# Performance work log

Measured on AMD Instinct MI355X. Metric: run time of the kernel, lower is better.

## Reference

```python
import jax, jax.numpy as jnp
import numpy as np

B_, L_, D_, R_, N_ = 8, 1024, 512, 32, 16  # batch, seq(in_channels), dim(=dim_inner), dt_rank, d_state


def setup_inputs() -> dict:
    key = jax.random.key(0)
    ks = jax.random.split(key, 8)
    s = lambda k, shape, scale: jax.random.normal(k, shape, dtype=jnp.float32) * scale
    inv = D_ ** -0.5
    return {
        "x": jax.random.uniform(ks[0], (B_, L_, D_), dtype=jnp.float32),
        "W1": s(ks[1], (D_, D_), inv), "b1": jnp.zeros((D_,), jnp.float32),
        "W2": s(ks[2], (D_, D_), inv), "b2": jnp.zeros((D_,), jnp.float32),
        "Wout": s(ks[3], (D_, D_), inv), "bout": jnp.zeros((D_,), jnp.float32),
        "conv_w": s(ks[4], (L_, L_, 3), (3 * L_) ** -0.5),  # Conv1d(L_, L_, k=3) weight (O,I,W)
        "conv_b": jnp.zeros((L_,), jnp.float32),
        "W_dbc": s(ks[5], (R_ + 2 * N_, D_), inv),          # deltaBC projection (no bias)
        "W_dt": s(ks[6], (D_, R_), R_ ** -0.5),             # dt_proj weight
        "b_dt": jnp.zeros((D_,), jnp.float32),
        "A_log": jnp.log(jnp.tile(jnp.arange(1, N_ + 1, dtype=jnp.float32), (D_, 1))),  # (D, N)
        "Dp": jnp.ones((D_,), jnp.float32),
    }


def _silu(v):
    return v * jax.nn.sigmoid(v)


def _selective_scan(u, delta, A, Bm, Cm, Dp):
    # u, delta: (b, l, d); A: (d, n); Bm, Cm: (b, l, n); Dp: (d,)
    dA = jnp.exp(jnp.einsum('bld,dn->bldn', delta, A))          # (b,l,d,n)
    dBu = jnp.einsum('bld,bln,bld->bldn', delta, Bm, u)          # (b,l,d,n)

    def step(h, inp):
        dA_t, dBu_t, C_t = inp                                   # (b,d,n),(b,d,n),(b,n)
        h = dA_t * h + dBu_t
        return h, jnp.einsum('bdn,bn->bd', h, C_t)

    h0 = jnp.zeros((u.shape[0], u.shape[2], A.shape[1]), u.dtype)
    _, ys = jax.lax.scan(step, h0, (dA.transpose(1, 0, 2, 3), dBu.transpose(1, 0, 2, 3), Cm.transpose(1, 0, 2)))
    return ys.transpose(1, 0, 2) + u * Dp                        # (b,l,d)


def reference(x, W1, b1, W2, b2, Wout, bout, conv_w, conv_b, W_dbc, W_dt, b_dt, A_log, Dp):
    skip = x
    x1 = x @ W1.T + b1                                            # proj_one
    x2 = x @ W2.T + b2                                            # proj_two
    # Conv1d over channel axis = L_ (dim 1), spatial axis = D_ (dim 2)
    x1 = jax.lax.conv_general_dilated(x1, conv_w, window_strides=(1,), padding=((1, 1),),
                                      dimension_numbers=('NCW', 'OIW', 'NCW')) + conv_b[None, :, None]
    x1 = _silu(x1)
    # SSM (zeta-style): deltaBC -> split -> dt_proj -> softplus -> selective scan
    dbc = x1 @ W_dbc.T                                            # (b,l,R+2N)
    delta = jax.nn.softplus(dbc[..., :R_] @ W_dt.T + b_dt)        # (b,l,d)
    Bm, Cm = dbc[..., R_:R_ + N_], dbc[..., R_ + N_:]
    A = -jnp.exp(A_log)
    y = _selective_scan(x1, delta, A, Bm, Cm, Dp)
    out = y * _silu(x2) + skip
    return out @ Wout.T + bout
```

## Files before the change

kernel.cpp:

```cpp
#include <hip/hip_runtime.h>
#include <hip/hip_bf16.h>

typedef __hip_bfloat16 bf16;
typedef __bf16 bf16x8 __attribute__((ext_vector_type(8)));
typedef float f32x4 __attribute__((ext_vector_type(4)));

static_assert(sizeof(bf16) == 2, "bf16 must be 2 bytes");

#define NC 32
#define CH 32
#define X1TP_BSTRIDE (514L * 1024)

__device__ __forceinline__ float silu_f(float v) { return v / (1.0f + __expf(-v)); }

__device__ __forceinline__ void gload16(const bf16* g, bf16* l) {
  __builtin_amdgcn_global_load_lds((const __attribute__((address_space(1))) void*)g,
                                   (__attribute__((address_space(3))) void*)l,
                                   16, 0, 0);
}

template <int N> __device__ __forceinline__ void wait_vm() {
  static_assert(N == 0 || N == 4 || N == 8 || N == 12, "add case");
  if constexpr (N == 0)       asm volatile("s_waitcnt vmcnt(0)" ::: "memory");
  else if constexpr (N == 4)  asm volatile("s_waitcnt vmcnt(4)" ::: "memory");
  else if constexpr (N == 8)  asm volatile("s_waitcnt vmcnt(8)" ::: "memory");
  else if constexpr (N == 12) asm volatile("s_waitcnt vmcnt(12)" ::: "memory");
}

__global__ __launch_bounds__(256) void prep_all(
    const float* __restrict__ x, const float* __restrict__ W1,
    const float* __restrict__ W2, const float* __restrict__ Wout,
    const float* __restrict__ Wdbc, const float* __restrict__ convw,
    bf16* __restrict__ xb, bf16* __restrict__ w1b, bf16* __restrict__ w2b,
    bf16* __restrict__ woutb, bf16* __restrict__ wdbcb,
    bf16* __restrict__ cws, bf16* __restrict__ x1tp) {
  const int gid = blockIdx.x * 256 + threadIdx.x;
  auto cvt4 = [](const float* src, bf16* dst, long q) {
    float4 v = *reinterpret_cast<const float4*>(src + q * 4);
    ushort4 s;
    s.x = __builtin_bit_cast(unsigned short, __float2bfloat16(v.x));
    s.y = __builtin_bit_cast(unsigned short, __float2bfloat16(v.y));
    s.z = __builtin_bit_cast(unsigned short, __float2bfloat16(v.z));
    s.w = __builtin_bit_cast(unsigned short, __float2bfloat16(v.w));
    *reinterpret_cast<ushort4*>(dst + q * 4) = s;
  };
  if (gid < 1048576) {
    cvt4(x, xb, gid);
  } else if (gid < 1114112) {
    cvt4(W1, w1b, gid - 1048576);
  } else if (gid < 1179648) {
    cvt4(W2, w2b, gid - 1114112);
  } else if (gid < 1245184) {
    cvt4(Wout, woutb, gid - 1179648);
  } else if (gid < 1253376) {
    cvt4(Wdbc, wdbcb, gid - 1245184);
  } else if (gid < 2301952) {
    long idx = gid - 1253376;
    int o = (int)(idx >> 10), i = (int)(idx & 1023);
    float a = convw[idx * 3], b = convw[idx * 3 + 1], c = convw[idx * 3 + 2];
    cws[(long)o * 3072 + i]        = __float2bfloat16(a);
    cws[(long)o * 3072 + 1024 + i] = __float2bfloat16(b);
    cws[(long)o * 3072 + 2048 + i] = __float2bfloat16(c);
  } else {
    int e = gid - 2301952;
    int b = e >> 11, rem = e & 2047;
    int r = rem >> 10, ii = rem & 1023;
    x1tp[(long)b * X1TP_BSTRIDE + (long)r * (513 * 1024) + ii] = __float2bfloat16(0.f);
  }
}

template <int EPI, int BM, int BN, int CONVB, int NBUF>
__device__ __forceinline__ void gemm_body(const bf16* __restrict__ A,
                                          const bf16* __restrict__ Bw,
                                          const float* __restrict__ bias,
                                          float* __restrict__ outf,
                                          bf16* __restrict__ outb,
                                          int M, int N, int K, int lda, int ldb,
                                          long sAz, long sBz, long sOz,
                                          int bx, int by, int z,
                                          bf16* As, bf16* Bs) {
  constexpr int BK = 64;
  constexpr int MI = BM / 32, WNF = BN / 32;
  constexpr int APW = BM / 32, BPW = BN / 32;
  constexpr int IPW = APW + BPW;

  const int tid = threadIdx.x;
  const int w = tid >> 6, l = tid & 63;
  const int wm = w >> 1, wn = w & 1;
  const int m0 = bx * BM, n0 = by * BN;
  const bf16* Ab = A + (long)z * sAz + (long)m0 * lda;
  const bf16* Bb = Bw + (long)z * sBz;

  const int lrow = l >> 3;
  const int lcol = (((l & 7) ^ (l >> 3)) << 3);

  auto stage = [&](int buf, int k0) {
#pragma unroll
    for (int j = 0; j < APW; ++j) {
      int iss = w * APW + j;
      int row = iss * 8 + lrow;
      gload16(Ab + (long)row * lda + k0 + lcol, &As[buf * BM * 64 + iss * 512]);
    }
#pragma unroll
    for (int j = 0; j < BPW; ++j) {
      int iss = w * BPW + j;
      int row = iss * 8 + lrow;
      const bf16* src;
      if (CONVB) src = Bb + (long)(n0 + row + (k0 >> 10)) * 1024 + (k0 & 1023) + lcol;
      else       src = Bb + (long)(n0 + row) * ldb + k0 + lcol;
      gload16(src, &Bs[buf * BN * 64 + iss * 512]);
    }
  };

  f32x4 acc[MI][WNF] = {};
  const int nt = K / BK;
  const int lr = l & 15;
  const int lko = (l >> 4) * 8;
  const int xorm = (lr & 7) << 3;

#pragma unroll
  for (int s = 0; s < NBUF - 1; ++s) stage(s, s * BK);
  for (int t = 0; t < nt; ++t) {
    const int cur = t % NBUF;
    if (t + NBUF - 1 < nt) {
      stage((t + NBUF - 1) % NBUF, (t + NBUF - 1) * BK);
      wait_vm<(NBUF - 1) * IPW>();
    } else {
      wait_vm<0>();
    }
    __builtin_amdgcn_s_barrier();
    __builtin_amdgcn_sched_barrier(0);
#pragma unroll
    for (int kk = 0; kk < 2; ++kk) {
      const int col = (lko + kk * 32) ^ xorm;
      bf16x8 af[MI], bfg[WNF];
#pragma unroll
      for (int mi = 0; mi < MI; ++mi)
        af[mi] = *reinterpret_cast<const bf16x8*>(
            &As[cur * BM * 64 + (wm * (BM / 2) + mi * 16 + lr) * 64 + col]);
#pragma unroll
      for (int ni = 0; ni < WNF; ++ni)
        bfg[ni] = *reinterpret_cast<const bf16x8*>(
            &Bs[cur * BN * 64 + (wn * (BN / 2) + ni * 16 + lr) * 64 + col]);
#pragma unroll
      for (int mi = 0; mi < MI; ++mi)
#pragma unroll
        for (int ni = 0; ni < WNF; ++ni)
          acc[mi][ni] = __builtin_amdgcn_mfma_f32_16x16x32_bf16(af[mi], bfg[ni], acc[mi][ni], 0, 0, 0);
    }
    __builtin_amdgcn_sched_barrier(0);
    __builtin_amdgcn_s_barrier();
  }

  const int lq = l >> 4;
#pragma unroll
  for (int mi = 0; mi < MI; ++mi) {
#pragma unroll
    for (int ni = 0; ni < WNF; ++ni) {
#pragma unroll
      for (int j = 0; j < 4; ++j) {
        int m = m0 + wm * (BM / 2) + mi * 16 + lq * 4 + j;
        int n = n0 + wn * (BN / 2) + ni * 16 + lr;
        float v = acc[mi][ni][j];
        if (EPI == 2) {
          v += bias[m];
          (outb + (long)z * sOz)[(long)m * N + n] = __float2bfloat16(silu_f(v));
        } else if (EPI == 3) {
          outf[(long)m * N + n] = v;
        } else if (EPI == 4) {
          v += bias[n];
          outf[(long)m * N + n] = v;
        } else if (EPI == 5) {
          v += bias[m];
          int b = n >> 10, li = n & 1023;
          outb[(long)b * X1TP_BSTRIDE + (long)(m + 1) * 1024 + li] = __float2bfloat16(v);
        } else {
          v += bias[n];
          outb[(long)m * N + n] = __float2bfloat16(silu_f(v));
        }
      }
    }
  }
}

template <int EPI, int BM, int BN, int CONVB, int NBUF, int GX, int GY>
__global__ __launch_bounds__(256) void gemm_nt(const bf16* __restrict__ A,
                                               const bf16* __restrict__ Bw,
                                               const float* __restrict__ bias,
                                               float* __restrict__ outf,
                                               bf16* __restrict__ outb,
                                               int M, int N, int K, int lda, int ldb,
                                               long sAz, long sBz, long sOz) {
  __shared__ __align__(16) bf16 As[NBUF * BM * 64];
  __shared__ __align__(16) bf16 Bs[NBUF * BN * 64];
  const int bid = (blockIdx.x & 7) * ((int)gridDim.x >> 3) + (blockIdx.x >> 3);
  const int by = bid % GY;
  const int bx = (bid / GY) % GX;
  const int z  = bid / (GX * GY);
  gemm_body<EPI, BM, BN, CONVB, NBUF>(A, Bw, bias, outf, outb, M, N, K, lda, ldb,
                                      sAz, sBz, sOz, bx, by, z, As, Bs);
}

__global__ __launch_bounds__(256) void gemm_dual(
    const bf16* __restrict__ w1b, const bf16* __restrict__ xb1,
    const float* __restrict__ b1, bf16* __restrict__ x1tp,
    const bf16* __restrict__ xb2, const bf16* __restrict__ w2b,
    const float* __restrict__ b2, bf16* __restrict__ x2g) {
  __shared__ __align__(16) bf16 As[2 * 128 * 64];
  __shared__ __align__(16) bf16 Bs[2 * 128 * 64];
  int bid = (blockIdx.x & 7) * 64 + (blockIdx.x >> 3);
  if (bid < 256) {
    int by = bid & 63, bx = bid >> 6;
    gemm_body<5, 128, 128, 0, 2>(w1b, xb1, b1, nullptr, x1tp, 512, 8192, 512, 512, 512,
                                 0, 0, 0, bx, by, 0, As, Bs);
  } else {
    bid -= 256;
    int by = bid & 3, bx = bid >> 2;
    gemm_body<6, 128, 128, 0, 2>(xb2, w2b, b2, nullptr, x2g, 8192, 512, 512, 512, 512,
                                 0, 0, 0, bx, by, 0, As, Bs);
  }
}

__global__ __launch_bounds__(256) void scan_p1(const bf16* __restrict__ u_bf,
                                               const float* __restrict__ dbc,
                                               const float* __restrict__ W_dt,
                                               const float* __restrict__ b_dt,
                                               const float* __restrict__ A_log,
                                               float* __restrict__ P,
                                               float* __restrict__ Q) {
  const int tid = threadIdx.x;
  const int d = blockIdx.x * 256 + tid;
  const int c = blockIdx.y, b = blockIdx.z;
  __shared__ float sD[CH][64];
  for (int i = tid; i < CH * 64; i += 256) {
    int tt = i >> 6, j = i & 63;
    sD[tt][j] = dbc[((long)b * 1024 + c * CH + tt) * 64 + j];
  }
  __syncthreads();
  float wdt[32];
#pragma unroll
  for (int r = 0; r < 32; r += 4) {
    float4 v = *reinterpret_cast<const float4*>(&W_dt[(long)d * 32 + r]);
    wdt[r] = v.x; wdt[r + 1] = v.y; wdt[r + 2] = v.z; wdt[r + 3] = v.w;
  }
  const float bd = b_dt[d];
  float Adn[16];
#pragma unroll
  for (int n = 0; n < 16; ++n) Adn[n] = -__expf(A_log[d * 16 + n]);
  float p[16], q[16];
#pragma unroll
  for (int n = 0; n < 16; ++n) { p[n] = 1.f; q[n] = 0.f; }
  const long rowb = (long)b * 1024 + c * CH;
  for (int tt = 0; tt < CH; ++tt) {
    float a = bd;
#pragma unroll
    for (int r = 0; r < 32; ++r) a = fmaf(sD[tt][r], wdt[r], a);
    float dv = fmaxf(a, 0.f) + log1pf(__expf(-fabsf(a)));
    float uv = __bfloat162float(u_bf[(rowb + tt) * 512 + d]);
    float s = dv * uv;
#pragma unroll
    for (int n = 0; n < 16; ++n) {
      float dA = __expf(dv * Adn[n]);
      p[n] *= dA;
      q[n] = fmaf(dA, q[n], s * sD[tt][32 + n]);
    }
  }
  float* Pp = P + ((long)b * NC + c) * 8192 + (long)d * 16;
  float* Qp = Q + ((long)b * NC + c) * 8192 + (long)d * 16;
#pragma unroll
  for (int n4 = 0; n4 < 4; ++n4) {
    *reinterpret_cast<float4*>(Pp + n4 * 4) = make_float4(p[n4*4], p[n4*4+1], p[n4*4+2], p[n4*4+3]);
    *reinterpret_cast<float4*>(Qp + n4 * 4) = make_float4(q[n4*4], q[n4*4+1], q[n4*4+2], q[n4*4+3]);
  }
}

__global__ __launch_bounds__(256) void scan_p2(const float* __restrict__ P,
                                               const float* __restrict__ Q,
                                               float* __restrict__ Hin) {
  const int dn = blockIdx.x * 256 + threadIdx.x;
  const int b = blockIdx.y;
  float h = 0.f;
#pragma unroll 4
  for (int c = 0; c < NC; ++c) {
    long idx = ((long)b * NC + c) * 8192 + dn;
    Hin[idx] = h;
    h = fmaf(P[idx], h, Q[idx]);
  }
}

__global__ __launch_bounds__(256) void scan_p3(const bf16* __restrict__ u_bf,
                                               const float* __restrict__ dbc,
                                               const float* __restrict__ W_dt,
                                               const float* __restrict__ b_dt,
                                               const float* __restrict__ A_log,
                                               const float* __restrict__ Dp,
                                               const bf16* __restrict__ x2g,
                                               const bf16* __restrict__ xres,
                                               const float* __restrict__ Hin,
                                               bf16* __restrict__ zb) {
  const int tid = threadIdx.x;
  const int d = blockIdx.x * 256 + tid;
  const int c = blockIdx.y, b = blockIdx.z;
  __shared__ float sD[CH][64];
  for (int i = tid; i < CH * 64; i += 256) {
    int tt = i >> 6, j = i & 63;
    sD[tt][j] = dbc[((long)b * 1024 + c * CH + tt) * 64 + j];
  }
  __syncthreads();
  float wdt[32];
#pragma unroll
  for (int r = 0; r < 32; r += 4) {
    float4 v = *reinterpret_cast<const float4*>(&W_dt[(long)d * 32 + r]);
    wdt[r] = v.x; wdt[r + 1] = v.y; wdt[r + 2] = v.z; wdt[r + 3] = v.w;
  }
  const float bd = b_dt[d];
  float Adn[16];
#pragma unroll
  for (int n = 0; n < 16; ++n) Adn[n] = -__expf(A_log[d * 16 + n]);
  float h[16];
  const float* Hp = Hin + ((long)b * NC + c) * 8192 + (long)d * 16;
#pragma unroll
  for (int n4 = 0; n4 < 4; ++n4) {
    float4 v = *reinterpret_cast<const float4*>(Hp + n4 * 4);
    h[n4*4] = v.x; h[n4*4+1] = v.y; h[n4*4+2] = v.z; h[n4*4+3] = v.w;
  }
  const float Dpv = Dp[d];
  const long rowb = (long)b * 1024 + c * CH;
  for (int tt = 0; tt < CH; ++tt) {
    long off = (rowb + tt) * 512 + d;
    float a = bd;
#pragma unroll
    for (int r = 0; r < 32; ++r) a = fmaf(sD[tt][r], wdt[r], a);
    float dv = fmaxf(a, 0.f) + log1pf(__expf(-fabsf(a)));
    float uv = __bfloat162float(u_bf[off]);
    float s = dv * uv;
    float y = uv * Dpv;
#pragma unroll
    for (int n = 0; n < 16; ++n) {
      float dA = __expf(dv * Adn[n]);
      h[n] = fmaf(dA, h[n], s * sD[tt][32 + n]);
      y = fmaf(h[n], sD[tt][48 + n], y);
    }
    float gate = __bfloat162float(x2g[off]);
    float xv = __bfloat162float(xres[off]);
    zb[off] = __float2bfloat16(fmaf(y, gate, xv));
  }
}

extern "C" void kernel_launch(void* const* d_in, const int* in_sizes, int n_in,
                              void* d_out, int out_size, void* d_ws, size_t ws_size,
                              hipStream_t stream) {
  (void)in_sizes; (void)n_in; (void)out_size; (void)ws_size;
  const float* x    = (const float*)d_in[0];
  const float* W1   = (const float*)d_in[1];
  const float* b1   = (const float*)d_in[2];
  const float* W2   = (const float*)d_in[3];
  const float* b2   = (const float*)d_in[4];
  const float* Wout = (const float*)d_in[5];
  const float* bout = (const float*)d_in[6];
  const float* convw = (const float*)d_in[7];
  const float* convb = (const float*)d_in[8];
  const float* Wdbc = (const float*)d_in[9];
  const float* Wdt  = (const float*)d_in[10];
  const float* bdt  = (const float*)d_in[11];
  const float* Alog = (const float*)d_in[12];
  const float* Dp   = (const float*)d_in[13];
  float* out = (float*)d_out;

  char* ws = (char*)d_ws;
  size_t off = 0;
  auto alloc = [&](size_t bytes) { void* p = ws + off; off += (bytes + 255) & ~(size_t)255; return p; };
  bf16* xb     = (bf16*)alloc(8192L * 512 * 2);
  bf16* w1b    = (bf16*)alloc(512L * 512 * 2);
  bf16* w2b    = (bf16*)alloc(512L * 512 * 2);
  bf16* woutb  = (bf16*)alloc(512L * 512 * 2);
  bf16* wdbcb  = (bf16*)alloc(64L * 512 * 2);
  bf16* cws    = (bf16*)alloc(1024L * 3072 * 2);
  bf16* x1tp   = (bf16*)alloc(8L * X1TP_BSTRIDE * 2);
  bf16* x2g    = (bf16*)alloc(8192L * 512 * 2);
  bf16* x1s    = (bf16*)alloc(8192L * 512 * 2);
  float* dbc   = (float*)alloc(8192L * 64 * 4);
  float* P     = (float*)alloc(8L * NC * 8192 * 4);
  float* Q     = (float*)alloc(8L * NC * 8192 * 4);
  float* Hin   = (float*)alloc(8L * NC * 8192 * 4);
  bf16* zb = xb;

  prep_all<<<9056, 256, 0, stream>>>(x, W1, W2, Wout, Wdbc, convw,
                                     xb, w1b, w2b, woutb, wdbcb, cws, x1tp);
  gemm_dual<<<512, 256, 0, stream>>>(w1b, xb, b1, x1tp, xb, w2b, b2, x2g);
  gemm_nt<2, 64, 128, 1, 3, 16, 4><<<512, 256, 0, stream>>>(
      cws, x1tp, convb, nullptr, x1s, 1024, 512, 3072, 3072, 0,
      0, X1TP_BSTRIDE, 1024L * 512);
  gemm_nt<3, 64, 64, 0, 3, 128, 1><<<128, 256, 0, stream>>>(
      x1s, wdbcb, nullptr, dbc, nullptr, 8192, 64, 512, 512, 512, 0, 0, 0);
  scan_p1<<<dim3(2, NC, 8), 256, 0, stream>>>(x1s, dbc, Wdt, bdt, Alog, P, Q);
  scan_p2<<<dim3(32, 8, 1), 256, 0, stream>>>(P, Q, Hin);
  scan_p3<<<dim3(2, NC, 8), 256, 0, stream>>>(x1s, dbc, Wdt, bdt, Alog, Dp, x2g, xb, Hin, zb);
  gemm_nt<4, 64, 128, 0, 3, 128, 4><<<512, 256, 0, stream>>>(
      zb, woutb, bout, out, nullptr, 8192, 512, 512, 512, 512, 0, 0, 0);
}
```

Measured before the change: 167.8 us.

## Single-barrier GEMM pipeline, smaller dual-GEMM tiles, split scan state across thread pairs

The GEMM main loop now waits for the current stage, uses one barrier, and only then issues the next prefetch. This removes the second barrier per K-step, and the prefetch is safe because the buffer it overwrites was last read before that barrier. The dual projection GEMM moves from 128x128 tiles with two buffers to 64x128 tiles with three buffers, doubling its grid to 1024 blocks. The scan kernels split the 16 state channels across two lanes per d, which doubles their blocks; the y partial sums are combined with a shuffle. The trade-off is that each thread pair now duplicates the delta and softplus computation.

```diff
diff --git a/kernel.cpp b/kernel.cpp
--- a/kernel.cpp
+++ b/kernel.cpp
@@ -20,9 +20,10 @@
 }
 
 template <int N> __device__ __forceinline__ void wait_vm() {
-  static_assert(N == 0 || N == 4 || N == 8 || N == 12, "add case");
+  static_assert(N == 0 || N == 4 || N == 6 || N == 8 || N == 12, "add case");
   if constexpr (N == 0)       asm volatile("s_waitcnt vmcnt(0)" ::: "memory");
   else if constexpr (N == 4)  asm volatile("s_waitcnt vmcnt(4)" ::: "memory");
+  else if constexpr (N == 6)  asm volatile("s_waitcnt vmcnt(6)" ::: "memory");
   else if constexpr (N == 8)  asm volatile("s_waitcnt vmcnt(8)" ::: "memory");
   else if constexpr (N == 12) asm volatile("s_waitcnt vmcnt(12)" ::: "memory");
 }
@@ -122,14 +123,11 @@
   for (int s = 0; s < NBUF - 1; ++s) stage(s, s * BK);
   for (int t = 0; t < nt; ++t) {
     const int cur = t % NBUF;
-    if (t + NBUF - 1 < nt) {
-      stage((t + NBUF - 1) % NBUF, (t + NBUF - 1) * BK);
-      wait_vm<(NBUF - 1) * IPW>();
-    } else {
-      wait_vm<0>();
-    }
+    if (t + 1 < nt) wait_vm<(NBUF - 2) * IPW>();
+    else            wait_vm<0>();
     __builtin_amdgcn_s_barrier();
     __builtin_amdgcn_sched_barrier(0);
+    if (t + NBUF - 1 < nt) stage((t + NBUF - 1) % NBUF, (t + NBUF - 1) * BK);
 #pragma unroll
     for (int kk = 0; kk < 2; ++kk) {
       const int col = (lko + kk * 32) ^ xorm;
@@ -148,8 +146,6 @@
         for (int ni = 0; ni < WNF; ++ni)
           acc[mi][ni] = __builtin_amdgcn_mfma_f32_16x16x32_bf16(af[mi], bfg[ni], acc[mi][ni], 0, 0, 0);
     }
-    __builtin_amdgcn_sched_barrier(0);
-    __builtin_amdgcn_s_barrier();
   }
 
   const int lq = l >> 4;
@@ -206,18 +202,18 @@
     const float* __restrict__ b1, bf16* __restrict__ x1tp,
     const bf16* __restrict__ xb2, const bf16* __restrict__ w2b,
     const float* __restrict__ b2, bf16* __restrict__ x2g) {
-  __shared__ __align__(16) bf16 As[2 * 128 * 64];
-  __shared__ __align__(16) bf16 Bs[2 * 128 * 64];
-  int bid = (blockIdx.x & 7) * 64 + (blockIdx.x >> 3);
-  if (bid < 256) {
-    int by = bid & 63, bx = bid >> 6;
-    gemm_body<5, 128, 128, 0, 2>(w1b, xb1, b1, nullptr, x1tp, 512, 8192, 512, 512, 512,
-                                 0, 0, 0, bx, by, 0, As, Bs);
+  __shared__ __align__(16) bf16 As[3 * 64 * 64];
+  __shared__ __align__(16) bf16 Bs[3 * 128 * 64];
+  int bid = (blockIdx.x & 7) * 128 + (blockIdx.x >> 3);
+  if (bid < 512) {
+    int by = bid % 64, bx = (bid / 64) % 8;
+    gemm_body<5, 64, 128, 0, 3>(w1b, xb1, b1, nullptr, x1tp, 512, 8192, 512, 512, 512,
+                                0, 0, 0, bx, by, 0, As, Bs);
   } else {
-    bid -= 256;
-    int by = bid & 3, bx = bid >> 2;
-    gemm_body<6, 128, 128, 0, 2>(xb2, w2b, b2, nullptr, x2g, 8192, 512, 512, 512, 512,
-                                 0, 0, 0, bx, by, 0, As, Bs);
+    bid -= 512;
+    int by = bid % 4, bx = (bid / 4) % 128;
+    gemm_body<6, 64, 128, 0, 3>(xb2, w2b, b2, nullptr, x2g, 8192, 512, 512, 512, 512,
+                                0, 0, 0, bx, by, 0, As, Bs);
   }
 }
 
@@ -229,7 +225,8 @@
                                                float* __restrict__ P,
                                                float* __restrict__ Q) {
   const int tid = threadIdx.x;
-  const int d = blockIdx.x * 256 + tid;
+  const int nh = tid & 1;
+  const int d = blockIdx.x * 128 + (tid >> 1);
   const int c = blockIdx.y, b = blockIdx.z;
   __shared__ float sD[CH][64];
   for (int i = tid; i < CH * 64; i += 256) {
@@ -244,12 +241,12 @@
     wdt[r] = v.x; wdt[r + 1] = v.y; wdt[r + 2] = v.z; wdt[r + 3] = v.w;
   }
   const float bd = b_dt[d];
-  float Adn[16];
-#pragma unroll
-  for (int n = 0; n < 16; ++n) Adn[n] = -__expf(A_log[d * 16 + n]);
-  float p[16], q[16];
-#pragma unroll
-  for (int n = 0; n < 16; ++n) { p[n] = 1.f; q[n] = 0.f; }
+  float Adn[8];
+#pragma unroll
+  for (int n = 0; n < 8; ++n) Adn[n] = -__expf(A_log[d * 16 + nh * 8 + n]);
+  float p[8], q[8];
+#pragma unroll
+  for (int n = 0; n < 8; ++n) { p[n] = 1.f; q[n] = 0.f; }
   const long rowb = (long)b * 1024 + c * CH;
   for (int tt = 0; tt < CH; ++tt) {
     float a = bd;
@@ -259,19 +256,18 @@
     float uv = __bfloat162float(u_bf[(rowb + tt) * 512 + d]);
     float s = dv * uv;
 #pragma unroll
-    for (int n = 0; n < 16; ++n) {
+    for (int n = 0; n < 8; ++n) {
       float dA = __expf(dv * Adn[n]);
       p[n] *= dA;
-      q[n] = fmaf(dA, q[n], s * sD[tt][32 + n]);
-    }
-  }
-  float* Pp = P + ((long)b * NC + c) * 8192 + (long)d * 16;
-  float* Qp = Q + ((long)b * NC + c) * 8192 + (long)d * 16;
-#pragma unroll
-  for (int n4 = 0; n4 < 4; ++n4) {
-    *reinterpret_cast<float4*>(Pp + n4 * 4) = make_float4(p[n4*4], p[n4*4+1], p[n4*4+2], p[n4*4+3]);
-    *reinterpret_cast<float4*>(Qp + n4 * 4) = make_float4(q[n4*4], q[n4*4+1], q[n4*4+2], q[n4*4+3]);
-  }
+      q[n] = fmaf(dA, q[n], s * sD[tt][32 + nh * 8 + n]);
+    }
+  }
+  float* Pp = P + ((long)b * NC + c) * 8192 + (long)d * 16 + nh * 8;
+  float* Qp = Q + ((long)b * NC + c) * 8192 + (long)d * 16 + nh * 8;
+  *reinterpret_cast<float4*>(Pp)     = make_float4(p[0], p[1], p[2], p[3]);
+  *reinterpret_cast<float4*>(Pp + 4) = make_float4(p[4], p[5], p[6], p[7]);
+  *reinterpret_cast<float4*>(Qp)     = make_float4(q[0], q[1], q[2], q[3]);
+  *reinterpret_cast<float4*>(Qp + 4) = make_float4(q[4], q[5], q[6], q[7]);
 }
 
 __global__ __launch_bounds__(256) void scan_p2(const float* __restrict__ P,
@@ -299,7 +295,8 @@
                                                const float* __restrict__ Hin,
                                                bf16* __restrict__ zb) {
   const int tid = threadIdx.x;
-  const int d = blockIdx.x * 256 + tid;
+  const int nh = tid & 1;
+  const int d = blockIdx.x * 128 + (tid >> 1);
   const int c = blockIdx.y, b = blockIdx.z;
   __shared__ float sD[CH][64];
   for (int i = tid; i < CH * 64; i += 256) {
@@ -314,15 +311,16 @@
     wdt[r] = v.x; wdt[r + 1] = v.y; wdt[r + 2] = v.z; wdt[r + 3] = v.w;
   }
   const float bd = b_dt[d];
-  float Adn[16];
-#pragma unroll
-  for (int n = 0; n < 16; ++n) Adn[n] = -__expf(A_log[d * 16 + n]);
-  float h[16];
-  const float* Hp = Hin + ((long)b * NC + c) * 8192 + (long)d * 16;
-#pragma unroll
-  for (int n4 = 0; n4 < 4; ++n4) {
-    float4 v = *reinterpret_cast<const float4*>(Hp + n4 * 4);
-    h[n4*4] = v.x; h[n4*4+1] = v.y; h[n4*4+2] = v.z; h[n4*4+3] = v.w;
+  float Adn[8];
+#pragma unroll
+  for (int n = 0; n < 8; ++n) Adn[n] = -__expf(A_log[d * 16 + nh * 8 + n]);
+  float h[8];
+  const float* Hp = Hin + ((long)b * NC + c) * 8192 + (long)d * 16 + nh * 8;
+  {
+    float4 v0 = *reinterpret_cast<const float4*>(Hp);
+    float4 v1 = *reinterpret_cast<const float4*>(Hp + 4);
+    h[0] = v0.x; h[1] = v0.y; h[2] = v0.z; h[3] = v0.w;
+    h[4] = v1.x; h[5] = v1.y; h[6] = v1.z; h[7] = v1.w;
   }
   const float Dpv = Dp[d];
   const long rowb = (long)b * 1024 + c * CH;
@@ -334,16 +332,17 @@
     float dv = fmaxf(a, 0.f) + log1pf(__expf(-fabsf(a)));
     float uv = __bfloat162float(u_bf[off]);
     float s = dv * uv;
-    float y = uv * Dpv;
-#pragma unroll
-    for (int n = 0; n < 16; ++n) {
+    float y = nh ? 0.f : uv * Dpv;
+#pragma unroll
+    for (int n = 0; n < 8; ++n) {
       float dA = __expf(dv * Adn[n]);
-      h[n] = fmaf(dA, h[n], s * sD[tt][32 + n]);
-      y = fmaf(h[n], sD[tt][48 + n], y);
-    }
+      h[n] = fmaf(dA, h[n], s * sD[tt][32 + nh * 8 + n]);
+      y = fmaf(h[n], sD[tt][48 + nh * 8 + n], y);
+    }
+    y += __shfl_xor(y, 1);
     float gate = __bfloat162float(x2g[off]);
     float xv = __bfloat162float(xres[off]);
-    zb[off] = __float2bfloat16(fmaf(y, gate, xv));
+    if (nh == 0) zb[off] = __float2bfloat16(fmaf(y, gate, xv));
   }
 }
 
@@ -387,15 +386,15 @@
 
   prep_all<<<9056, 256, 0, stream>>>(x, W1, W2, Wout, Wdbc, convw,
                                      xb, w1b, w2b, woutb, wdbcb, cws, x1tp);
-  gemm_dual<<<512, 256, 0, stream>>>(w1b, xb, b1, x1tp, xb, w2b, b2, x2g);
+  gemm_dual<<<1024, 256, 0, stream>>>(w1b, xb, b1, x1tp, xb, w2b, b2, x2g);
   gemm_nt<2, 64, 128, 1, 3, 16, 4><<<512, 256, 0, stream>>>(
       cws, x1tp, convb, nullptr, x1s, 1024, 512, 3072, 3072, 0,
       0, X1TP_BSTRIDE, 1024L * 512);
   gemm_nt<3, 64, 64, 0, 3, 128, 1><<<128, 256, 0, stream>>>(
       x1s, wdbcb, nullptr, dbc, nullptr, 8192, 64, 512, 512, 512, 0, 0, 0);
-  scan_p1<<<dim3(2, NC, 8), 256, 0, stream>>>(x1s, dbc, Wdt, bdt, Alog, P, Q);
+  scan_p1<<<dim3(4, NC, 8), 256, 0, stream>>>(x1s, dbc, Wdt, bdt, Alog, P, Q);
   scan_p2<<<dim3(32, 8, 1), 256, 0, stream>>>(P, Q, Hin);
-  scan_p3<<<dim3(2, NC, 8), 256, 0, stream>>>(x1s, dbc, Wdt, bdt, Alog, Dp, x2g, xb, Hin, zb);
+  scan_p3<<<dim3(4, NC, 8), 256, 0, stream>>>(x1s, dbc, Wdt, bdt, Alog, Dp, x2g, xb, Hin, zb);
   gemm_nt<4, 64, 128, 0, 3, 128, 4><<<512, 256, 0, stream>>>(
       zb, woutb, bout, out, nullptr, 8192, 512, 512, 512, 512, 0, 0, 0);
 }
```

Measured after the change: 205.9 us. 1.23x slower.

## Restructure GEMM pipeline to one barrier, shrink tiles, cache delta for scan

Applied to the files above, without the earlier changes.

The GEMM main loop now waits for the current stage, barriers once, then issues the next prefetch before computing. This drops the second barrier per K-step. All GEMM launches move to smaller 64x64 tiles with more blocks and a three-buffer pipeline in gemm_dual, to raise occupancy and spread work over more CUs. scan_p1 now writes the softplus delta to a new fp32 workspace buffer, and scan_p3 reads it back instead of recomputing the 32-wide dt projection and softplus. That trades extra global memory traffic (16 MB written and read) for less compute.

```diff
diff --git a/kernel.cpp b/kernel.cpp
--- a/kernel.cpp
+++ b/kernel.cpp
@@ -20,9 +20,10 @@
 }
 
 template <int N> __device__ __forceinline__ void wait_vm() {
-  static_assert(N == 0 || N == 4 || N == 8 || N == 12, "add case");
+  static_assert(N == 0 || N == 4 || N == 6 || N == 8 || N == 12, "add case");
   if constexpr (N == 0)       asm volatile("s_waitcnt vmcnt(0)" ::: "memory");
   else if constexpr (N == 4)  asm volatile("s_waitcnt vmcnt(4)" ::: "memory");
+  else if constexpr (N == 6)  asm volatile("s_waitcnt vmcnt(6)" ::: "memory");
   else if constexpr (N == 8)  asm volatile("s_waitcnt vmcnt(8)" ::: "memory");
   else if constexpr (N == 12) asm volatile("s_waitcnt vmcnt(12)" ::: "memory");
 }
@@ -122,14 +123,11 @@
   for (int s = 0; s < NBUF - 1; ++s) stage(s, s * BK);
   for (int t = 0; t < nt; ++t) {
     const int cur = t % NBUF;
-    if (t + NBUF - 1 < nt) {
-      stage((t + NBUF - 1) % NBUF, (t + NBUF - 1) * BK);
-      wait_vm<(NBUF - 1) * IPW>();
-    } else {
-      wait_vm<0>();
-    }
+    if (t + 1 < nt) wait_vm<(NBUF - 2) * IPW>();
+    else            wait_vm<0>();
     __builtin_amdgcn_s_barrier();
     __builtin_amdgcn_sched_barrier(0);
+    if (t + NBUF - 1 < nt) stage((t + NBUF - 1) % NBUF, (t + NBUF - 1) * BK);
 #pragma unroll
     for (int kk = 0; kk < 2; ++kk) {
       const int col = (lko + kk * 32) ^ xorm;
@@ -148,8 +146,6 @@
         for (int ni = 0; ni < WNF; ++ni)
           acc[mi][ni] = __builtin_amdgcn_mfma_f32_16x16x32_bf16(af[mi], bfg[ni], acc[mi][ni], 0, 0, 0);
     }
-    __builtin_amdgcn_sched_barrier(0);
-    __builtin_amdgcn_s_barrier();
   }
 
   const int lq = l >> 4;
@@ -206,18 +202,18 @@
     const float* __restrict__ b1, bf16* __restrict__ x1tp,
     const bf16* __restrict__ xb2, const bf16* __restrict__ w2b,
     const float* __restrict__ b2, bf16* __restrict__ x2g) {
-  __shared__ __align__(16) bf16 As[2 * 128 * 64];
-  __shared__ __align__(16) bf16 Bs[2 * 128 * 64];
-  int bid = (blockIdx.x & 7) * 64 + (blockIdx.x >> 3);
-  if (bid < 256) {
-    int by = bid & 63, bx = bid >> 6;
-    gemm_body<5, 128, 128, 0, 2>(w1b, xb1, b1, nullptr, x1tp, 512, 8192, 512, 512, 512,
-                                 0, 0, 0, bx, by, 0, As, Bs);
+  __shared__ __align__(16) bf16 As[3 * 64 * 64];
+  __shared__ __align__(16) bf16 Bs[3 * 64 * 64];
+  int bid = (blockIdx.x & 7) * 256 + (blockIdx.x >> 3);
+  if (bid < 1024) {
+    int by = bid % 128, bx = (bid / 128) & 7;
+    gemm_body<5, 64, 64, 0, 3>(w1b, xb1, b1, nullptr, x1tp, 512, 8192, 512, 512, 512,
+                               0, 0, 0, bx, by, 0, As, Bs);
   } else {
-    bid -= 256;
-    int by = bid & 3, bx = bid >> 2;
-    gemm_body<6, 128, 128, 0, 2>(xb2, w2b, b2, nullptr, x2g, 8192, 512, 512, 512, 512,
-                                 0, 0, 0, bx, by, 0, As, Bs);
+    bid -= 1024;
+    int by = bid & 7, bx = (bid / 8) & 127;
+    gemm_body<6, 64, 64, 0, 3>(xb2, w2b, b2, nullptr, x2g, 8192, 512, 512, 512, 512,
+                               0, 0, 0, bx, by, 0, As, Bs);
   }
 }
 
@@ -227,13 +223,14 @@
                                                const float* __restrict__ b_dt,
                                                const float* __restrict__ A_log,
                                                float* __restrict__ P,
-                                               float* __restrict__ Q) {
+                                               float* __restrict__ Q,
+                                               float* __restrict__ delta) {
   const int tid = threadIdx.x;
   const int d = blockIdx.x * 256 + tid;
   const int c = blockIdx.y, b = blockIdx.z;
-  __shared__ float sD[CH][64];
-  for (int i = tid; i < CH * 64; i += 256) {
-    int tt = i >> 6, j = i & 63;
+  __shared__ float sD[CH][48];
+  for (int i = tid; i < CH * 48; i += 256) {
+    int tt = i / 48, j = i % 48;
     sD[tt][j] = dbc[((long)b * 1024 + c * CH + tt) * 64 + j];
   }
   __syncthreads();
@@ -252,11 +249,13 @@
   for (int n = 0; n < 16; ++n) { p[n] = 1.f; q[n] = 0.f; }
   const long rowb = (long)b * 1024 + c * CH;
   for (int tt = 0; tt < CH; ++tt) {
+    long off = (rowb + tt) * 512 + d;
     float a = bd;
 #pragma unroll
     for (int r = 0; r < 32; ++r) a = fmaf(sD[tt][r], wdt[r], a);
     float dv = fmaxf(a, 0.f) + log1pf(__expf(-fabsf(a)));
-    float uv = __bfloat162float(u_bf[(rowb + tt) * 512 + d]);
+    delta[off] = dv;
+    float uv = __bfloat162float(u_bf[off]);
     float s = dv * uv;
 #pragma unroll
     for (int n = 0; n < 16; ++n) {
@@ -290,8 +289,7 @@
 
 __global__ __launch_bounds__(256) void scan_p3(const bf16* __restrict__ u_bf,
                                                const float* __restrict__ dbc,
-                                               const float* __restrict__ W_dt,
-                                               const float* __restrict__ b_dt,
+                                               const float* __restrict__ delta,
                                                const float* __restrict__ A_log,
                                                const float* __restrict__ Dp,
                                                const bf16* __restrict__ x2g,
@@ -301,19 +299,12 @@
   const int tid = threadIdx.x;
   const int d = blockIdx.x * 256 + tid;
   const int c = blockIdx.y, b = blockIdx.z;
-  __shared__ float sD[CH][64];
-  for (int i = tid; i < CH * 64; i += 256) {
-    int tt = i >> 6, j = i & 63;
-    sD[tt][j] = dbc[((long)b * 1024 + c * CH + tt) * 64 + j];
+  __shared__ float sD[CH][32];
+  for (int i = tid; i < CH * 32; i += 256) {
+    int tt = i >> 5, j = i & 31;
+    sD[tt][j] = dbc[((long)b * 1024 + c * CH + tt) * 64 + 32 + j];
   }
   __syncthreads();
-  float wdt[32];
-#pragma unroll
-  for (int r = 0; r < 32; r += 4) {
-    float4 v = *reinterpret_cast<const float4*>(&W_dt[(long)d * 32 + r]);
-    wdt[r] = v.x; wdt[r + 1] = v.y; wdt[r + 2] = v.z; wdt[r + 3] = v.w;
-  }
-  const float bd = b_dt[d];
   float Adn[16];
 #pragma unroll
   for (int n = 0; n < 16; ++n) Adn[n] = -__expf(A_log[d * 16 + n]);
@@ -328,18 +319,15 @@
   const long rowb = (long)b * 1024 + c * CH;
   for (int tt = 0; tt < CH; ++tt) {
     long off = (rowb + tt) * 512 + d;
-    float a = bd;
-#pragma unroll
-    for (int r = 0; r < 32; ++r) a = fmaf(sD[tt][r], wdt[r], a);
-    float dv = fmaxf(a, 0.f) + log1pf(__expf(-fabsf(a)));
+    float dv = delta[off];
     float uv = __bfloat162float(u_bf[off]);
     float s = dv * uv;
     float y = uv * Dpv;
 #pragma unroll
     for (int n = 0; n < 16; ++n) {
       float dA = __expf(dv * Adn[n]);
-      h[n] = fmaf(dA, h[n], s * sD[tt][32 + n]);
-      y = fmaf(h[n], sD[tt][48 + n], y);
+      h[n] = fmaf(dA, h[n], s * sD[tt][n]);
+      y = fmaf(h[n], sD[tt][16 + n], y);
     }
     float gate = __bfloat162float(x2g[off]);
     float xv = __bfloat162float(xres[off]);
@@ -380,6 +368,7 @@
   bf16* x2g    = (bf16*)alloc(8192L * 512 * 2);
   bf16* x1s    = (bf16*)alloc(8192L * 512 * 2);
   float* dbc   = (float*)alloc(8192L * 64 * 4);
+  float* delta = (float*)alloc(8192L * 512 * 4);
   float* P     = (float*)alloc(8L * NC * 8192 * 4);
   float* Q     = (float*)alloc(8L * NC * 8192 * 4);
   float* Hin   = (float*)alloc(8L * NC * 8192 * 4);
@@ -387,15 +376,15 @@
 
   prep_all<<<9056, 256, 0, stream>>>(x, W1, W2, Wout, Wdbc, convw,
                                      xb, w1b, w2b, woutb, wdbcb, cws, x1tp);
-  gemm_dual<<<512, 256, 0, stream>>>(w1b, xb, b1, x1tp, xb, w2b, b2, x2g);
-  gemm_nt<2, 64, 128, 1, 3, 16, 4><<<512, 256, 0, stream>>>(
+  gemm_dual<<<2048, 256, 0, stream>>>(w1b, xb, b1, x1tp, xb, w2b, b2, x2g);
+  gemm_nt<2, 64, 64, 1, 3, 16, 8><<<1024, 256, 0, stream>>>(
       cws, x1tp, convb, nullptr, x1s, 1024, 512, 3072, 3072, 0,
       0, X1TP_BSTRIDE, 1024L * 512);
   gemm_nt<3, 64, 64, 0, 3, 128, 1><<<128, 256, 0, stream>>>(
       x1s, wdbcb, nullptr, dbc, nullptr, 8192, 64, 512, 512, 512, 0, 0, 0);
-  scan_p1<<<dim3(2, NC, 8), 256, 0, stream>>>(x1s, dbc, Wdt, bdt, Alog, P, Q);
+  scan_p1<<<dim3(2, NC, 8), 256, 0, stream>>>(x1s, dbc, Wdt, bdt, Alog, P, Q, delta);
   scan_p2<<<dim3(32, 8, 1), 256, 0, stream>>>(P, Q, Hin);
-  scan_p3<<<dim3(2, NC, 8), 256, 0, stream>>>(x1s, dbc, Wdt, bdt, Alog, Dp, x2g, xb, Hin, zb);
-  gemm_nt<4, 64, 128, 0, 3, 128, 4><<<512, 256, 0, stream>>>(
+  scan_p3<<<dim3(2, NC, 8), 256, 0, stream>>>(x1s, dbc, delta, Alog, Dp, x2g, xb, Hin, zb);
+  gemm_nt<4, 64, 64, 0, 3, 128, 8><<<1024, 256, 0, stream>>>(
       zb, woutb, bout, out, nullptr, 8192, 512, 512, 512, 512, 0, 0, 0);
 }
```

New measurement: 189.2 us. 12.8% more time.
